# Performance work log

Hardware: AMD Instinct MI355X
Metric: run time of the kernel (lower is better)

## Reference

```python
import jax, jax.numpy as jnp
import numpy as np

B, C, P, H, W, S = 4, 256, 128, 56, 56, 5
EPS = 1e-5


def setup_inputs() -> dict:
    key = jax.random.key(0)
    ks = jax.random.split(key, 6)
    return {
        "x": jax.random.normal(ks[0], (B, C, H, W), jnp.float32),
        "Wt": jax.random.normal(ks[1], (P, C), jnp.float32) * 0.05,
        "Wp": jax.random.normal(ks[2], (P, C), jnp.float32) * 0.05,
        "Wg": jax.random.normal(ks[3], (S, P, C), jnp.float32) * 0.05,
        "W1": jax.random.normal(ks[4], (S, C, P), jnp.float32) * 0.05,
        "W2": jax.random.normal(ks[5], (S, C, P), jnp.float32) * 0.05,
        "gamma": jnp.ones((S, C), jnp.float32),
        "beta": jnp.zeros((S, C), jnp.float32),
    }


def _batchnorm(o, g, b):
    # training-mode BN over (batch, spatial); o: [b, C, n]
    mean = o.mean(axis=(0, 2), keepdims=True)
    var = ((o - mean) ** 2).mean(axis=(0, 2), keepdims=True)
    return (o - mean) * jax.lax.rsqrt(var + EPS) * g[None, :, None] + b[None, :, None]


def reference(x, Wt, Wp, Wg, W1, W2, gamma, beta):
    b, c, h, w = x.shape
    n = h * w
    xf = x.reshape(b, c, n)
    # 1x1 conv projections == channel matmuls
    t = jax.nn.relu(jnp.einsum('pc,bcn->bpn', Wt, xf))  # is_norm branch uses relu
    p = jax.nn.relu(jnp.einsum('pc,bcn->bpn', Wp, xf))
    att = jnp.einsum('bpi,bpj->bij', t, p)              # [b, n, n] affinity
    att = 0.5 * (att + jnp.swapaxes(att, 1, 2))         # is_sys symmetrization
    d = att.sum(axis=2)                                  # degree [b, n]
    d_safe = jnp.where(d != 0, d, 1.0)
    d_inv = jnp.where(d != 0, jax.lax.rsqrt(d_safe), 0.0)
    att = att * d_inv[:, None, :] * d_inv[:, :, None]    # D^-1/2 A D^-1/2
    out = xf
    for s in range(S):  # fixed small stage count
        g = jnp.einsum('pc,bcn->bpn', Wg[s], out)        # [b, P, n]
        ag = jnp.einsum('bij,bpj->bpi', att, g)          # att @ g over spatial
        o = jnp.einsum('cp,bpn->bcn', W1[s], ag) + jnp.einsum('cp,bpn->bcn', W2[s], g)
        out = _batchnorm(o, gamma[s], beta[s]) + out     # BN + residual
    return out.reshape(b, c, h, w)
```

## Files before the change

kernel.cpp:

```cpp
#include <hip/hip_runtime.h>

namespace {

constexpr int Bc = 4;
constexpr int Cc = 256;
constexpr int Pc = 128;
constexpr int Nc = 3136;
constexpr int Sc = 5;
constexpr int KSn = 7;
constexpr int KCH = 448;
constexpr float EPSc = 1e-5f;

typedef __attribute__((ext_vector_type(8))) short bf16x8;
typedef __attribute__((ext_vector_type(4))) float f32x4;
typedef __attribute__((ext_vector_type(8))) unsigned short u16x8;
typedef __attribute__((ext_vector_type(4))) unsigned short u16x4;

__device__ inline float bf2f(unsigned short u) {
    return __uint_as_float(((unsigned)u) << 16);
}
__device__ inline unsigned short f2bf(float f) {
    unsigned u = __float_as_uint(f);
    return (unsigned short)((u + 0x7FFFu + ((u >> 16) & 1u)) >> 16);
}

template <int EPI, int CMOUT, bool SPLITK, int BNSTAT, bool F32OUT>
__global__ __launch_bounds__(256) void mgemm(
    const unsigned short* __restrict__ A, int lda, long aB,
    const unsigned short* __restrict__ Bw, int ldb, long bB,
    unsigned short* __restrict__ outSM, int ldsm, long smB, long smSlice,
    unsigned short* __restrict__ outCM, long cmB,
    float* __restrict__ ps, float* __restrict__ ps2,
    int K, int kchunk, const float* __restrict__ dinv)
{
    constexpr int TBA = 64 * 64 * 2;
    constexpr int TBB = 128 * 64 * 2;
    constexpr int BUF = TBA + TBB;
    __shared__ __align__(16) char lds[2 * BUF];

    int b, kstart, kend;
    long smOff;
    if (SPLITK) {
        b = blockIdx.z & 3;
        int ks = blockIdx.z >> 2;
        kstart = ks * kchunk;
        kend = kstart + kchunk;
        smOff = (long)ks * smSlice;
    } else {
        b = blockIdx.z; kstart = 0; kend = K; smOff = 0;
    }
    const int n0 = blockIdx.x * 128;
    const int m0 = blockIdx.y * 64;
    const int tid = threadIdx.x;
    const int w = tid >> 6, l = tid & 63;

    const unsigned short* Ab = A + (size_t)b * aB + (size_t)m0 * lda;
    const unsigned short* Bb = Bw + (size_t)b * bB + (size_t)n0 * ldb;

    const int srow = w * 8 + (l >> 3);
    const int gsw = ((l & 7) ^ (l >> 3)) * 8;

    f32x4 acc[4][2] = {};

    auto stage = [&](int buf, int k0) {
        char* base = lds + buf * BUF;
#pragma unroll
        for (int j = 0; j < 2; ++j) {
            __builtin_amdgcn_global_load_lds(
                (const __attribute__((address_space(1))) void*)
                    (Ab + (size_t)(j * 32 + srow) * lda + k0 + gsw),
                (__attribute__((address_space(3))) void*)(base + j * 4096 + w * 1024),
                16, 0, 0);
        }
#pragma unroll
        for (int j = 0; j < 4; ++j) {
            __builtin_amdgcn_global_load_lds(
                (const __attribute__((address_space(1))) void*)
                    (Bb + (size_t)(j * 32 + srow) * ldb + k0 + gsw),
                (__attribute__((address_space(3))) void*)(base + TBA + j * 4096 + w * 1024),
                16, 0, 0);
        }
    };

    auto compute = [&](int buf) {
        const char* base = lds + buf * BUF;
        const int lo = l & 15, gq = l >> 4;
#pragma unroll
        for (int kh = 0; kh < 2; ++kh) {
            const int lg = kh * 4 + gq;
            bf16x8 bf[2];
#pragma unroll
            for (int c = 0; c < 2; ++c) {
                int brow = w * 32 + c * 16 + lo;
                bf[c] = *(const bf16x8*)(base + TBA + brow * 128 + ((lg ^ (brow & 7)) << 4));
            }
#pragma unroll
            for (int r = 0; r < 4; ++r) {
                int row = r * 16 + lo;
                bf16x8 af = *(const bf16x8*)(base + row * 128 + ((lg ^ (row & 7)) << 4));
                acc[r][0] = __builtin_amdgcn_mfma_f32_16x16x32_bf16(af, bf[0], acc[r][0], 0, 0, 0);
                acc[r][1] = __builtin_amdgcn_mfma_f32_16x16x32_bf16(af, bf[1], acc[r][1], 0, 0, 0);
            }
        }
    };

    stage(0, kstart);
    __syncthreads();
    const int nst = (kend - kstart) >> 6;
    for (int s = 0; s < nst; ++s) {
        if (s + 1 < nst) stage((s + 1) & 1, kstart + ((s + 1) << 6));
        compute(s & 1);
        __syncthreads();
    }

    float* ot = (float*)lds;
    {
        const int lo = l & 15, gq = l >> 4;
#pragma unroll
        for (int r = 0; r < 4; ++r)
#pragma unroll
            for (int c = 0; c < 2; ++c)
#pragma unroll
                for (int j = 0; j < 4; ++j) {
                    float v = acc[r][c][j];
                    if (EPI == 1) v = fmaxf(v, 0.f);
                    ot[(r * 16 + gq * 4 + j) * 132 + w * 32 + c * 16 + lo] = v;
                }
    }
    __syncthreads();

    {
        const int r = tid >> 2, c0 = (tid & 3) * 32;
        if (F32OUT) {
            float* dst = (float*)outSM + (size_t)b * smB + smOff +
                         (size_t)(m0 + r) * ldsm + n0 + c0;
#pragma unroll
            for (int k = 0; k < 8; ++k) {
                float4 v;
                v.x = ot[r * 132 + c0 + 4 * k + 0];
                v.y = ot[r * 132 + c0 + 4 * k + 1];
                v.z = ot[r * 132 + c0 + 4 * k + 2];
                v.w = ot[r * 132 + c0 + 4 * k + 3];
                *(float4*)(dst + 4 * k) = v;
            }
        } else {
            float sc = 1.f;
            if (EPI == 2) sc = 0.5f * dinv[(size_t)b * Nc + m0 + r];
            unsigned short* dst = outSM + (size_t)b * smB + smOff +
                                  (size_t)(m0 + r) * ldsm + n0 + c0;
#pragma unroll
            for (int k = 0; k < 4; ++k) {
                u16x8 o;
#pragma unroll
                for (int j = 0; j < 8; ++j) {
                    float v = ot[r * 132 + c0 + 8 * k + j];
                    if (EPI == 2) v *= sc;
                    o[j] = f2bf(v);
                }
                *(u16x8*)(dst + 8 * k) = o;
            }
        }
    }

    if (CMOUT) {
        const int c = tid >> 1, r0 = (tid & 1) * 32;
        const float* dv = dinv + (size_t)b * Nc + m0 + r0;
        unsigned short* dst = outCM + (size_t)b * cmB + (size_t)(n0 + c) * Nc + m0 + r0;
#pragma unroll
        for (int k = 0; k < 4; ++k) {
            u16x8 o;
#pragma unroll
            for (int j = 0; j < 8; ++j) {
                float v = ot[(r0 + 8 * k + j) * 132 + c];
                if (CMOUT == 2) v *= dv[8 * k + j];
                o[j] = f2bf(v);
            }
            *(u16x8*)(dst + 8 * k) = o;
        }
    }

    if (BNSTAT) {
        float* p1 = (float*)(lds + 35840);
        float* p2 = p1 + 256;
        const int col = tid & 127, half = tid >> 7;
        float s = 0.f, s2 = 0.f;
#pragma unroll
        for (int i = 0; i < 32; ++i) {
            float v = ot[(half * 32 + i) * 132 + col];
            s += v;
            if (BNSTAT == 2) s2 = fmaf(v, v, s2);
        }
        p1[half * 128 + col] = s;
        if (BNSTAT == 2) p2[half * 128 + col] = s2;
        __syncthreads();
        if (tid < 128) {
            float a = p1[tid] + p1[128 + tid];
            size_t slot = ((size_t)b * 49 + blockIdx.y) * 256 + n0 + tid;
            ps[slot] = a;
            if (BNSTAT == 2) ps2[slot] = p2[tid] + p2[128 + tid];
        }
    }
}

__global__ __launch_bounds__(256) void cvtw_k(
    const float* __restrict__ Wt, const float* __restrict__ Wp,
    const float* __restrict__ Wg, const float* __restrict__ W1,
    const float* __restrict__ W2,
    unsigned short* __restrict__ Wcomb, unsigned short* __restrict__ Wgh,
    unsigned short* __restrict__ Wcat)
{
    size_t e = ((size_t)blockIdx.x * 256 + threadIdx.x) * 4;
    const float* src; unsigned short* dst;
    if (e < 32768)      { src = Wt + e;           dst = Wcomb + e; }
    else if (e < 65536) { src = Wp + (e - 32768); dst = Wcomb + e; }
    else if (e < 65536 + 163840) {
        size_t o = e - 65536; src = Wg + o; dst = Wgh + o;
    } else if (e < 65536 + 2 * 163840) {
        size_t o = e - 65536 - 163840; src = W1 + o;
        dst = Wcat + ((o >> 7) << 8) + (o & 127);
    } else {
        size_t o = e - 65536 - 327680; src = W2 + o;
        dst = Wcat + ((o >> 7) << 8) + 128 + (o & 127);
    }
    float4 v = *(const float4*)src;
    u16x4 t;
    t[0] = f2bf(v.x); t[1] = f2bf(v.y); t[2] = f2bf(v.z); t[3] = f2bf(v.w);
    *(u16x4*)dst = t;
}

__global__ __launch_bounds__(256) void xpin_k(
    const float* __restrict__ x, float* __restrict__ out_sm,
    unsigned short* __restrict__ outh)
{
    __shared__ float tb[64][65];
    int b = blockIdx.z, c0 = blockIdx.y * 64, n0 = blockIdx.x * 64;
    int t = threadIdx.x;
    {
        int ci = t >> 2, nb = (t & 3) * 16;
        const float* src = x + ((size_t)b * Cc + c0 + ci) * Nc + n0 + nb;
#pragma unroll
        for (int k = 0; k < 4; ++k) {
            float4 v = *(const float4*)(src + 4 * k);
            tb[ci][nb + 4 * k + 0] = v.x; tb[ci][nb + 4 * k + 1] = v.y;
            tb[ci][nb + 4 * k + 2] = v.z; tb[ci][nb + 4 * k + 3] = v.w;
        }
    }
    __syncthreads();
    {
        int r = t >> 2, cb = (t & 3) * 16;
        size_t off = ((size_t)b * Nc + n0 + r) * Cc + c0 + cb;
        float vv[16];
#pragma unroll
        for (int j = 0; j < 16; ++j) vv[j] = tb[cb + j][r];
        float* dst = out_sm + off;
#pragma unroll
        for (int k = 0; k < 4; ++k) {
            float4 v; v.x = vv[4*k]; v.y = vv[4*k+1]; v.z = vv[4*k+2]; v.w = vv[4*k+3];
            *(float4*)(dst + 4 * k) = v;
        }
        u16x8 h1, h2;
#pragma unroll
        for (int j = 0; j < 8; ++j) { h1[j] = f2bf(vv[j]); h2[j] = f2bf(vv[8 + j]); }
        unsigned short* dh = outh + off;
        *(u16x8*)dh = h1;
        *(u16x8*)(dh + 8) = h2;
    }
}

__global__ __launch_bounds__(256) void xpout_k(
    const float* __restrict__ out_sm, float* __restrict__ outp)
{
    __shared__ float tb[64][65];
    int b = blockIdx.z, c0 = blockIdx.y * 64, n0 = blockIdx.x * 64;
    int t = threadIdx.x;
    {
        int r = t >> 2, cb = (t & 3) * 16;
        const float* src = out_sm + ((size_t)b * Nc + n0 + r) * Cc + c0 + cb;
#pragma unroll
        for (int k = 0; k < 4; ++k) {
            float4 v = *(const float4*)(src + 4 * k);
            tb[r][cb + 4 * k + 0] = v.x; tb[r][cb + 4 * k + 1] = v.y;
            tb[r][cb + 4 * k + 2] = v.z; tb[r][cb + 4 * k + 3] = v.w;
        }
    }
    __syncthreads();
    {
        int c = t >> 2, rb = (t & 3) * 16;
        float vv[16];
#pragma unroll
        for (int j = 0; j < 16; ++j) vv[j] = tb[rb + j][c];
        float* dst = outp + ((size_t)b * Cc + c0 + c) * Nc + n0 + rb;
#pragma unroll
        for (int k = 0; k < 4; ++k) {
            float4 v; v.x = vv[4*k]; v.y = vv[4*k+1]; v.z = vv[4*k+2]; v.w = vv[4*k+3];
            *(float4*)(dst + 4 * k) = v;
        }
    }
}

__global__ __launch_bounds__(256) void dinv_k(
    const unsigned short* __restrict__ U, const float* __restrict__ rp,
    float* __restrict__ dinv)
{
    __shared__ float rsl[256];
    int b = blockIdx.y, tid = threadIdx.x;
    float s = 0.f;
    for (int j = 0; j < 49; ++j) s += rp[((size_t)b * 49 + j) * 256 + tid];
    rsl[tid ^ 128] = s;
    __syncthreads();
    int i = blockIdx.x * 256 + tid;
    if (i < Nc) {
        const unsigned short* row = U + ((size_t)b * Nc + i) * 256;
        float acc = 0.f;
        for (int q0 = 0; q0 < 256; q0 += 8) {
            u16x8 v = *(const u16x8*)(row + q0);
#pragma unroll
            for (int j = 0; j < 8; ++j) acc = fmaf(bf2f(v[j]), rsl[q0 + j], acc);
        }
        float d = 0.5f * acc;
        dinv[(size_t)b * Nc + i] = d > 0.f ? rsqrtf(d) : 0.f;
    }
}

__global__ __launch_bounds__(256) void redmst_k(
    const float* __restrict__ Cpart, unsigned short* __restrict__ MstT)
{
    int e8 = blockIdx.x * 256 + threadIdx.x;
    int bp = e8 >> 5, qc = e8 & 31;
    size_t dstOff = ((size_t)bp * 32 + qc) * 8;
    size_t srcOff = ((size_t)bp * 32 + (qc ^ 16)) * 8;
    float4 s0 = {0.f, 0.f, 0.f, 0.f}, s1 = {0.f, 0.f, 0.f, 0.f};
    for (int ks = 0; ks < KSn; ++ks) {
        const float* base = Cpart + (size_t)ks * (Bc * Pc * Cc) + srcOff;
        float4 v0 = *(const float4*)base;
        float4 v1 = *(const float4*)(base + 4);
        s0.x += v0.x; s0.y += v0.y; s0.z += v0.z; s0.w += v0.w;
        s1.x += v1.x; s1.y += v1.y; s1.z += v1.z; s1.w += v1.w;
    }
    u16x8 o;
    o[0] = f2bf(s0.x); o[1] = f2bf(s0.y); o[2] = f2bf(s0.z); o[3] = f2bf(s0.w);
    o[4] = f2bf(s1.x); o[5] = f2bf(s1.y); o[6] = f2bf(s1.z); o[7] = f2bf(s1.w);
    *(u16x8*)(MstT + dstOff) = o;
}

__global__ __launch_bounds__(256) void bnfin_k(
    const float* __restrict__ ps, const float* __restrict__ ps2,
    const float* __restrict__ gamma, const float* __restrict__ beta,
    float* __restrict__ scale, float* __restrict__ shift)
{
    __shared__ float l1[256], l2[256];
    int t = threadIdx.x;
    int c = blockIdx.x * 16 + (t & 15);
    int gl = t >> 4;
    float a = 0.f, a2 = 0.f;
    for (int g = gl; g < 196; g += 16) {
        a += ps[(size_t)g * 256 + c];
        a2 += ps2[(size_t)g * 256 + c];
    }
    l1[t] = a; l2[t] = a2;
    __syncthreads();
    if (gl == 0) {
#pragma unroll
        for (int j = 1; j < 16; ++j) {
            a += l1[j * 16 + (t & 15)];
            a2 += l2[j * 16 + (t & 15)];
        }
        const float inv = 1.f / (float)(Bc * Nc);
        float mean = a * inv;
        float var = a2 * inv - mean * mean;
        float sc = gamma[c] * rsqrtf(var + EPSc);
        scale[c] = sc;
        shift[c] = beta[c] - mean * sc;
    }
}

__global__ __launch_bounds__(256) void bnapp_k(
    const unsigned short* __restrict__ o, const float* __restrict__ scale,
    const float* __restrict__ shift, float* __restrict__ out_sm,
    unsigned short* __restrict__ outh)
{
    __shared__ float lsc[256], lsh[256];
    int t = threadIdx.x;
    lsc[t] = scale[t];
    lsh[t] = shift[t];
    __syncthreads();
    size_t e = ((size_t)blockIdx.x * 256 + t) * 8;
    int c8 = (int)(e & 255);
    u16x8 ov = *(const u16x8*)(o + e);
    float* op = out_sm + e;
    float4 o1 = *(float4*)op, o2 = *(float4*)(op + 4);
    float r[8];
#pragma unroll
    for (int j = 0; j < 8; ++j) r[j] = fmaf(bf2f(ov[j]), lsc[c8 + j], lsh[c8 + j]);
    o1.x += r[0]; o1.y += r[1]; o1.z += r[2]; o1.w += r[3];
    o2.x += r[4]; o2.y += r[5]; o2.z += r[6]; o2.w += r[7];
    *(float4*)op = o1;
    *(float4*)(op + 4) = o2;
    u16x8 hv;
    hv[0] = f2bf(o1.x); hv[1] = f2bf(o1.y); hv[2] = f2bf(o1.z); hv[3] = f2bf(o1.w);
    hv[4] = f2bf(o2.x); hv[5] = f2bf(o2.y); hv[6] = f2bf(o2.z); hv[7] = f2bf(o2.w);
    *(u16x8*)(outh + e) = hv;
}

}

extern "C" void kernel_launch(void* const* d_in, const int* in_sizes, int n_in,
                              void* d_out, int out_size, void* d_ws, size_t ws_size,
                              hipStream_t stream) {
    const float* x     = (const float*)d_in[0];
    const float* Wt    = (const float*)d_in[1];
    const float* Wp    = (const float*)d_in[2];
    const float* Wg    = (const float*)d_in[3];
    const float* W1    = (const float*)d_in[4];
    const float* W2    = (const float*)d_in[5];
    const float* gamma = (const float*)d_in[6];
    const float* beta  = (const float*)d_in[7];

    char* p = (char*)d_ws;
    auto alloc = [&](size_t bytes) { char* r = p; p += (bytes + 255) & ~(size_t)255; return r; };
    float*          out_sm = (float*)         alloc((size_t)Bc * Nc * Cc * 4);
    unsigned short* outh   = (unsigned short*)alloc((size_t)Bc * Nc * Cc * 2);
    unsigned short* U_sm   = (unsigned short*)alloc((size_t)Bc * Nc * 256 * 2);
    unsigned short* U_cm   = (unsigned short*)alloc((size_t)Bc * 256 * Nc * 2);
    unsigned short* agg    = (unsigned short*)alloc((size_t)Bc * Nc * 256 * 2);
    unsigned short* g_cmd  = (unsigned short*)alloc((size_t)Bc * Pc * Nc * 2);
    unsigned short* o_sm   = (unsigned short*)alloc((size_t)Bc * Nc * Cc * 2);
    float*          Cpart  = (float*)         alloc((size_t)KSn * Bc * Pc * Cc * 4);
    unsigned short* MstT   = (unsigned short*)alloc((size_t)Bc * Pc * Cc * 2);
    unsigned short* Wcomb  = (unsigned short*)alloc((size_t)Cc * Cc * 2);
    unsigned short* Wgh    = (unsigned short*)alloc((size_t)Sc * Pc * Cc * 2);
    unsigned short* Wcat   = (unsigned short*)alloc((size_t)Sc * Cc * 256 * 2);
    float*          rp     = (float*)         alloc((size_t)Bc * 49 * 256 * 4);
    float*          dinv   = (float*)         alloc((size_t)Bc * Nc * 4);
    float*          ps     = (float*)         alloc((size_t)196 * 256 * 4);
    float*          ps2    = (float*)         alloc((size_t)196 * 256 * 4);
    float*          scale  = (float*)         alloc(256 * 4);
    float*          shiftb = (float*)         alloc(256 * 4);

    const long NC256 = (long)Nc * 256;
    dim3 blk(256);

    cvtw_k<<<544, blk, 0, stream>>>(Wt, Wp, Wg, W1, W2, Wcomb, Wgh, Wcat);
    xpin_k<<<dim3(49, 4, Bc), blk, 0, stream>>>(x, out_sm, outh);

    mgemm<1, 1, false, 1, false><<<dim3(2, 49, Bc), blk, 0, stream>>>(
        outh, 256, NC256, Wcomb, 256, 0,
        U_sm, 256, NC256, 0, U_cm, (long)256 * Nc, rp, nullptr, 256, 0, nullptr);

    dinv_k<<<dim3(13, Bc), blk, 0, stream>>>(U_sm, rp, dinv);

    for (int s = 0; s < Sc; ++s) {
        mgemm<0, 2, false, 0, false><<<dim3(1, 49, Bc), blk, 0, stream>>>(
            outh, 256, NC256, Wgh + (size_t)s * Pc * Cc, 256, 0,
            agg + 128, 256, NC256, 0, g_cmd, (long)Pc * Nc, nullptr, nullptr,
            256, 0, dinv);
        mgemm<0, 0, true, 0, true><<<dim3(2, 2, KSn * Bc), blk, 0, stream>>>(
            g_cmd, Nc, (long)Pc * Nc, U_cm, Nc, (long)256 * Nc,
            (unsigned short*)Cpart, 256, (long)Pc * Cc, (long)Bc * Pc * Cc,
            nullptr, 0, nullptr, nullptr, Nc, KCH, nullptr);
        redmst_k<<<64, blk, 0, stream>>>(Cpart, MstT);
        mgemm<2, 0, false, 0, false><<<dim3(1, 49, Bc), blk, 0, stream>>>(
            U_sm, 256, NC256, MstT, 256, (long)Pc * Cc,
            agg, 256, NC256, 0, nullptr, 0, nullptr, nullptr, 256, 0, dinv);
        mgemm<0, 0, false, 2, false><<<dim3(2, 49, Bc), blk, 0, stream>>>(
            agg, 256, NC256, Wcat + (size_t)s * Cc * 256, 256, 0,
            o_sm, 256, NC256, 0, nullptr, 0, ps, ps2, 256, 0, nullptr);
        bnfin_k<<<16, blk, 0, stream>>>(ps, ps2, gamma + s * Cc, beta + s * Cc,
                                        scale, shiftb);
        bnapp_k<<<1568, blk, 0, stream>>>(o_sm, scale, shiftb, out_sm, outh);
    }

    xpout_k<<<dim3(49, 4, Bc), blk, 0, stream>>>(out_sm, (float*)d_out);
}
```

Measured before the change: 280.0 us.

## Fuse BN-apply into next stage GEMM prologue, pad N, use 128-row tiles

Removes the standalone BN-apply kernel. The scale, shift and residual add now happen in the next stage's g-projection GEMM, which loads o and the residual, writes the updated residual and stages the bf16 A tile into LDS itself. The final stage's BN is folded into the output transpose. The spatial dimension is padded to 3200 so tiles divide evenly, the split-K count drops from 7 to 5, and the wide GEMMs use 128-row tiles to halve the grid and amortize B loads. In exchange, padding adds some wasted work, and the fused prologue puts synchronous global loads in the GEMM pipeline.

```diff
diff --git a/kernel.cpp b/kernel.cpp
--- a/kernel.cpp
+++ b/kernel.cpp
@@ -5,10 +5,11 @@
 constexpr int Bc = 4;
 constexpr int Cc = 256;
 constexpr int Pc = 128;
-constexpr int Nc = 3136;
+constexpr int NcT = 3136;
+constexpr int Np = 3200;
 constexpr int Sc = 5;
-constexpr int KSn = 7;
-constexpr int KCH = 448;
+constexpr int KSn = 5;
+constexpr int KCH = 640;
 constexpr float EPSc = 1e-5f;
 
 typedef __attribute__((ext_vector_type(8))) short bf16x8;
@@ -24,19 +25,24 @@
     return (unsigned short)((u + 0x7FFFu + ((u >> 16) & 1u)) >> 16);
 }
 
-template <int EPI, int CMOUT, bool SPLITK, int BNSTAT, bool F32OUT>
+template <int MT, int EPI, int CMOUT, bool SPLITK, int BNSTAT, bool F32OUT,
+          bool FUSEBN>
 __global__ __launch_bounds__(256) void mgemm(
     const unsigned short* __restrict__ A, int lda, long aB,
     const unsigned short* __restrict__ Bw, int ldb, long bB,
     unsigned short* __restrict__ outSM, int ldsm, long smB, long smSlice,
     unsigned short* __restrict__ outCM, long cmB,
     float* __restrict__ ps, float* __restrict__ ps2,
-    int K, int kchunk, const float* __restrict__ dinv)
-{
-    constexpr int TBA = 64 * 64 * 2;
+    int K, int kchunk, const float* __restrict__ dinv,
+    const unsigned short* __restrict__ oin, const float* __restrict__ bnsc,
+    const float* __restrict__ bnsh, float* __restrict__ resid)
+{
+    constexpr int TBA = MT * 64 * 2;
     constexpr int TBB = 128 * 64 * 2;
     constexpr int BUF = TBA + TBB;
-    __shared__ __align__(16) char lds[2 * BUF];
+    constexpr int OTB = MT * 132 * 4;
+    constexpr int LDSZ = (2 * BUF > OTB + 2048) ? 2 * BUF : (OTB + 2048);
+    __shared__ __align__(16) char lds[LDSZ];
 
     int b, kstart, kend;
     long smOff;
@@ -50,35 +56,87 @@
         b = blockIdx.z; kstart = 0; kend = K; smOff = 0;
     }
     const int n0 = blockIdx.x * 128;
-    const int m0 = blockIdx.y * 64;
+    const int m0 = blockIdx.y * MT;
     const int tid = threadIdx.x;
     const int w = tid >> 6, l = tid & 63;
 
     const unsigned short* Ab = A + (size_t)b * aB + (size_t)m0 * lda;
     const unsigned short* Bb = Bw + (size_t)b * bB + (size_t)n0 * ldb;
 
-    const int srow = w * 8 + (l >> 3);
-    const int gsw = ((l & 7) ^ (l >> 3)) * 8;
-
-    f32x4 acc[4][2] = {};
-
-    auto stage = [&](int buf, int k0) {
+    const int srow8 = tid >> 3;
+    const int sgran = tid & 7;
+    const int sswz = (sgran ^ (srow8 & 7)) * 8;
+    constexpr int AR = MT / 32;
+
+    constexpr int WC = (MT == 128) ? 2 : 4;
+    constexpr int NB = 128 / WC / 16;
+    const int wr = w / WC, wc = w % WC;
+
+    f32x4 acc[4][NB] = {};
+    float fup[AR][8];
+
+    auto stageA = [&](int buf, int k0) {
         char* base = lds + buf * BUF;
 #pragma unroll
-        for (int j = 0; j < 2; ++j) {
+        for (int j = 0; j < AR; ++j)
             __builtin_amdgcn_global_load_lds(
                 (const __attribute__((address_space(1))) void*)
-                    (Ab + (size_t)(j * 32 + srow) * lda + k0 + gsw),
-                (__attribute__((address_space(3))) void*)(base + j * 4096 + w * 1024),
+                    (Ab + (size_t)(j * 32 + srow8) * lda + k0 + sswz),
+                (__attribute__((address_space(3))) void*)(base + j * 4096 + tid * 16),
                 16, 0, 0);
-        }
-#pragma unroll
-        for (int j = 0; j < 4; ++j) {
+    };
+    auto stageB = [&](int buf, int k0) {
+        char* base = lds + buf * BUF + TBA;
+#pragma unroll
+        for (int j = 0; j < 4; ++j)
             __builtin_amdgcn_global_load_lds(
                 (const __attribute__((address_space(1))) void*)
-                    (Bb + (size_t)(j * 32 + srow) * ldb + k0 + gsw),
-                (__attribute__((address_space(3))) void*)(base + TBA + j * 4096 + w * 1024),
+                    (Bb + (size_t)(j * 32 + srow8) * ldb + k0 + sswz),
+                (__attribute__((address_space(3))) void*)(base + j * 4096 + tid * 16),
                 16, 0, 0);
+    };
+    auto fbLoad = [&](int k0) {
+        const float* scp = bnsc + k0 + sgran * 8;
+        const float* shp = bnsh + k0 + sgran * 8;
+        float4 s0 = *(const float4*)scp, s1 = *(const float4*)(scp + 4);
+        float4 h0 = *(const float4*)shp, h1 = *(const float4*)(shp + 4);
+#pragma unroll
+        for (int j = 0; j < AR; ++j) {
+            int row = j * 32 + srow8;
+            int n = m0 + row;
+            size_t off = ((size_t)b * Np + n) * 256 + k0 + sgran * 8;
+            if (n < NcT) {
+                u16x8 ov = *(const u16x8*)(oin + off);
+                float4 r0 = *(const float4*)(resid + off);
+                float4 r1 = *(const float4*)(resid + off + 4);
+                fup[j][0] = r0.x + fmaf(bf2f(ov[0]), s0.x, h0.x);
+                fup[j][1] = r0.y + fmaf(bf2f(ov[1]), s0.y, h0.y);
+                fup[j][2] = r0.z + fmaf(bf2f(ov[2]), s0.z, h0.z);
+                fup[j][3] = r0.w + fmaf(bf2f(ov[3]), s0.w, h0.w);
+                fup[j][4] = r1.x + fmaf(bf2f(ov[4]), s1.x, h1.x);
+                fup[j][5] = r1.y + fmaf(bf2f(ov[5]), s1.y, h1.y);
+                fup[j][6] = r1.z + fmaf(bf2f(ov[6]), s1.z, h1.z);
+                fup[j][7] = r1.w + fmaf(bf2f(ov[7]), s1.w, h1.w);
+            } else {
+#pragma unroll
+                for (int i = 0; i < 8; ++i) fup[j][i] = 0.f;
+            }
+            float4 w0, w1;
+            w0.x = fup[j][0]; w0.y = fup[j][1]; w0.z = fup[j][2]; w0.w = fup[j][3];
+            w1.x = fup[j][4]; w1.y = fup[j][5]; w1.z = fup[j][6]; w1.w = fup[j][7];
+            *(float4*)(resid + off) = w0;
+            *(float4*)(resid + off + 4) = w1;
+        }
+    };
+    auto fbWrite = [&](int buf) {
+        char* base = lds + buf * BUF;
+#pragma unroll
+        for (int j = 0; j < AR; ++j) {
+            int row = j * 32 + srow8;
+            u16x8 hv;
+#pragma unroll
+            for (int i = 0; i < 8; ++i) hv[i] = f2bf(fup[j][i]);
+            *(u16x8*)(base + row * 128 + ((sgran ^ (row & 7)) << 4)) = hv;
         }
     };
 
@@ -88,29 +146,53 @@
 #pragma unroll
         for (int kh = 0; kh < 2; ++kh) {
             const int lg = kh * 4 + gq;
-            bf16x8 bf[2];
-#pragma unroll
-            for (int c = 0; c < 2; ++c) {
-                int brow = w * 32 + c * 16 + lo;
-                bf[c] = *(const bf16x8*)(base + TBA + brow * 128 + ((lg ^ (brow & 7)) << 4));
+            bf16x8 bf[NB];
+#pragma unroll
+            for (int c = 0; c < NB; ++c) {
+                int brow = wc * (16 * NB) + c * 16 + lo;
+                bf[c] = *(const bf16x8*)(base + TBA + brow * 128 +
+                                         ((lg ^ (brow & 7)) << 4));
             }
 #pragma unroll
             for (int r = 0; r < 4; ++r) {
-                int row = r * 16 + lo;
-                bf16x8 af = *(const bf16x8*)(base + row * 128 + ((lg ^ (row & 7)) << 4));
-                acc[r][0] = __builtin_amdgcn_mfma_f32_16x16x32_bf16(af, bf[0], acc[r][0], 0, 0, 0);
-                acc[r][1] = __builtin_amdgcn_mfma_f32_16x16x32_bf16(af, bf[1], acc[r][1], 0, 0, 0);
+                int arow = wr * 64 + r * 16 + lo;
+                bf16x8 af = *(const bf16x8*)(base + arow * 128 +
+                                             ((lg ^ (arow & 7)) << 4));
+#pragma unroll
+                for (int c = 0; c < NB; ++c)
+                    acc[r][c] = __builtin_amdgcn_mfma_f32_16x16x32_bf16(
+                        af, bf[c], acc[r][c], 0, 0, 0);
             }
         }
     };
 
-    stage(0, kstart);
-    __syncthreads();
     const int nst = (kend - kstart) >> 6;
-    for (int s = 0; s < nst; ++s) {
-        if (s + 1 < nst) stage((s + 1) & 1, kstart + ((s + 1) << 6));
-        compute(s & 1);
+    if constexpr (FUSEBN) {
+        fbLoad(kstart);
+        fbWrite(0);
+        stageB(0, kstart);
         __syncthreads();
+        for (int s = 0; s < nst; ++s) {
+            if (s + 1 < nst) {
+                fbLoad(kstart + ((s + 1) << 6));
+                stageB((s + 1) & 1, kstart + ((s + 1) << 6));
+            }
+            compute(s & 1);
+            if (s + 1 < nst) fbWrite((s + 1) & 1);
+            __syncthreads();
+        }
+    } else {
+        stageA(0, kstart);
+        stageB(0, kstart);
+        __syncthreads();
+        for (int s = 0; s < nst; ++s) {
+            if (s + 1 < nst) {
+                stageA((s + 1) & 1, kstart + ((s + 1) << 6));
+                stageB((s + 1) & 1, kstart + ((s + 1) << 6));
+            }
+            compute(s & 1);
+            __syncthreads();
+        }
     }
 
     float* ot = (float*)lds;
@@ -119,23 +201,26 @@
 #pragma unroll
         for (int r = 0; r < 4; ++r)
 #pragma unroll
-            for (int c = 0; c < 2; ++c)
+            for (int c = 0; c < NB; ++c)
 #pragma unroll
                 for (int j = 0; j < 4; ++j) {
                     float v = acc[r][c][j];
                     if (EPI == 1) v = fmaxf(v, 0.f);
-                    ot[(r * 16 + gq * 4 + j) * 132 + w * 32 + c * 16 + lo] = v;
+                    ot[(wr * 64 + r * 16 + gq * 4 + j) * 132 +
+                       wc * (16 * NB) + c * 16 + lo] = v;
                 }
     }
     __syncthreads();
 
     {
-        const int r = tid >> 2, c0 = (tid & 3) * 32;
+        constexpr int TPR = 256 / MT;
+        const int r = tid / TPR;
+        const int c0 = (tid % TPR) * (MT / 2);
         if (F32OUT) {
             float* dst = (float*)outSM + (size_t)b * smB + smOff +
                          (size_t)(m0 + r) * ldsm + n0 + c0;
 #pragma unroll
-            for (int k = 0; k < 8; ++k) {
+            for (int k = 0; k < MT / 8; ++k) {
                 float4 v;
                 v.x = ot[r * 132 + c0 + 4 * k + 0];
                 v.y = ot[r * 132 + c0 + 4 * k + 1];
@@ -145,11 +230,11 @@
             }
         } else {
             float sc = 1.f;
-            if (EPI == 2) sc = 0.5f * dinv[(size_t)b * Nc + m0 + r];
+            if (EPI == 2) sc = 0.5f * dinv[(size_t)b * Np + m0 + r];
             unsigned short* dst = outSM + (size_t)b * smB + smOff +
                                   (size_t)(m0 + r) * ldsm + n0 + c0;
 #pragma unroll
-            for (int k = 0; k < 4; ++k) {
+            for (int k = 0; k < MT / 16; ++k) {
                 u16x8 o;
 #pragma unroll
                 for (int j = 0; j < 8; ++j) {
@@ -163,11 +248,12 @@
     }
 
     if (CMOUT) {
-        const int c = tid >> 1, r0 = (tid & 1) * 32;
-        const float* dv = dinv + (size_t)b * Nc + m0 + r0;
-        unsigned short* dst = outCM + (size_t)b * cmB + (size_t)(n0 + c) * Nc + m0 + r0;
-#pragma unroll
-        for (int k = 0; k < 4; ++k) {
+        const int c = tid >> 1, r0 = (tid & 1) * (MT / 2);
+        const float* dv = dinv + (size_t)b * Np + m0 + r0;
+        unsigned short* dst = outCM + (size_t)b * cmB + (size_t)(n0 + c) * Np +
+                              m0 + r0;
+#pragma unroll
+        for (int k = 0; k < MT / 16; ++k) {
             u16x8 o;
 #pragma unroll
             for (int j = 0; j < 8; ++j) {
@@ -180,13 +266,13 @@
     }
 
     if (BNSTAT) {
-        float* p1 = (float*)(lds + 35840);
+        float* p1 = (float*)(lds + OTB);
         float* p2 = p1 + 256;
         const int col = tid & 127, half = tid >> 7;
         float s = 0.f, s2 = 0.f;
 #pragma unroll
-        for (int i = 0; i < 32; ++i) {
-            float v = ot[(half * 32 + i) * 132 + col];
+        for (int i = 0; i < MT / 2; ++i) {
+            float v = ot[(half * (MT / 2) + i) * 132 + col];
             s += v;
             if (BNSTAT == 2) s2 = fmaf(v, v, s2);
         }
@@ -195,7 +281,7 @@
         __syncthreads();
         if (tid < 128) {
             float a = p1[tid] + p1[128 + tid];
-            size_t slot = ((size_t)b * 49 + blockIdx.y) * 256 + n0 + tid;
+            size_t slot = ((size_t)b * gridDim.y + blockIdx.y) * 256 + n0 + tid;
             ps[slot] = a;
             if (BNSTAT == 2) ps2[slot] = p2[tid] + p2[128 + tid];
         }
@@ -235,9 +321,10 @@
     __shared__ float tb[64][65];
     int b = blockIdx.z, c0 = blockIdx.y * 64, n0 = blockIdx.x * 64;
     int t = threadIdx.x;
-    {
+    const bool pad = (n0 >= NcT);
+    if (!pad) {
         int ci = t >> 2, nb = (t & 3) * 16;
-        const float* src = x + ((size_t)b * Cc + c0 + ci) * Nc + n0 + nb;
+        const float* src = x + ((size_t)b * Cc + c0 + ci) * NcT + n0 + nb;
 #pragma unroll
         for (int k = 0; k < 4; ++k) {
             float4 v = *(const float4*)(src + 4 * k);
@@ -246,41 +333,52 @@
         }
     }
     __syncthreads();
+    int r = t >> 2, cb = (t & 3) * 16;
+    size_t off = ((size_t)b * Np + n0 + r) * 256 + c0 + cb;
+    float vv[16];
+#pragma unroll
+    for (int j = 0; j < 16; ++j) vv[j] = pad ? 0.f : tb[cb + j][r];
+    float* dst = out_sm + off;
+#pragma unroll
+    for (int k = 0; k < 4; ++k) {
+        float4 v; v.x = vv[4*k]; v.y = vv[4*k+1]; v.z = vv[4*k+2]; v.w = vv[4*k+3];
+        *(float4*)(dst + 4 * k) = v;
+    }
+    u16x8 h1, h2;
+#pragma unroll
+    for (int j = 0; j < 8; ++j) { h1[j] = f2bf(vv[j]); h2[j] = f2bf(vv[8 + j]); }
+    unsigned short* dh = outh + off;
+    *(u16x8*)dh = h1;
+    *(u16x8*)(dh + 8) = h2;
+}
+
+__global__ __launch_bounds__(256) void xpoutbn_k(
+    const float* __restrict__ out_sm, const unsigned short* __restrict__ oin,
+    const float* __restrict__ scale, const float* __restrict__ shift,
+    float* __restrict__ outp)
+{
+    __shared__ float tb[64][65];
+    __shared__ float lsc[64], lsh[64];
+    int b = blockIdx.z, c0 = blockIdx.y * 64, n0 = blockIdx.x * 64;
+    int t = threadIdx.x;
+    if (t < 64) { lsc[t] = scale[c0 + t]; lsh[t] = shift[c0 + t]; }
+    __syncthreads();
     {
         int r = t >> 2, cb = (t & 3) * 16;
-        size_t off = ((size_t)b * Nc + n0 + r) * Cc + c0 + cb;
-        float vv[16];
-#pragma unroll
-        for (int j = 0; j < 16; ++j) vv[j] = tb[cb + j][r];
-        float* dst = out_sm + off;
-#pragma unroll
-        for (int k = 0; k < 4; ++k) {
-            float4 v; v.x = vv[4*k]; v.y = vv[4*k+1]; v.z = vv[4*k+2]; v.w = vv[4*k+3];
-            *(float4*)(dst + 4 * k) = v;
-        }
-        u16x8 h1, h2;
-#pragma unroll
-        for (int j = 0; j < 8; ++j) { h1[j] = f2bf(vv[j]); h2[j] = f2bf(vv[8 + j]); }
-        unsigned short* dh = outh + off;
-        *(u16x8*)dh = h1;
-        *(u16x8*)(dh + 8) = h2;
-    }
-}
-
-__global__ __launch_bounds__(256) void xpout_k(
-    const float* __restrict__ out_sm, float* __restrict__ outp)
-{
-    __shared__ float tb[64][65];
-    int b = blockIdx.z, c0 = blockIdx.y * 64, n0 = blockIdx.x * 64;
-    int t = threadIdx.x;
-    {
-        int r = t >> 2, cb = (t & 3) * 16;
-        const float* src = out_sm + ((size_t)b * Nc + n0 + r) * Cc + c0 + cb;
-#pragma unroll
-        for (int k = 0; k < 4; ++k) {
-            float4 v = *(const float4*)(src + 4 * k);
-            tb[r][cb + 4 * k + 0] = v.x; tb[r][cb + 4 * k + 1] = v.y;
-            tb[r][cb + 4 * k + 2] = v.z; tb[r][cb + 4 * k + 3] = v.w;
+        size_t off = ((size_t)b * Np + n0 + r) * 256 + c0 + cb;
+#pragma unroll
+        for (int k = 0; k < 2; ++k) {
+            float4 a0 = *(const float4*)(out_sm + off + 8 * k);
+            float4 a1 = *(const float4*)(out_sm + off + 8 * k + 4);
+            u16x8 ov = *(const u16x8*)(oin + off + 8 * k);
+            tb[r][cb + 8*k + 0] = a0.x + fmaf(bf2f(ov[0]), lsc[cb + 8*k + 0], lsh[cb + 8*k + 0]);
+            tb[r][cb + 8*k + 1] = a0.y + fmaf(bf2f(ov[1]), lsc[cb + 8*k + 1], lsh[cb + 8*k + 1]);
+            tb[r][cb + 8*k + 2] = a0.z + fmaf(bf2f(ov[2]), lsc[cb + 8*k + 2], lsh[cb + 8*k + 2]);
+            tb[r][cb + 8*k + 3] = a0.w + fmaf(bf2f(ov[3]), lsc[cb + 8*k + 3], lsh[cb + 8*k + 3]);
+            tb[r][cb + 8*k + 4] = a1.x + fmaf(bf2f(ov[4]), lsc[cb + 8*k + 4], lsh[cb + 8*k + 4]);
+            tb[r][cb + 8*k + 5] = a1.y + fmaf(bf2f(ov[5]), lsc[cb + 8*k + 5], lsh[cb + 8*k + 5]);
+            tb[r][cb + 8*k + 6] = a1.z + fmaf(bf2f(ov[6]), lsc[cb + 8*k + 6], lsh[cb + 8*k + 6]);
+            tb[r][cb + 8*k + 7] = a1.w + fmaf(bf2f(ov[7]), lsc[cb + 8*k + 7], lsh[cb + 8*k + 7]);
         }
     }
     __syncthreads();
@@ -289,7 +387,7 @@
         float vv[16];
 #pragma unroll
         for (int j = 0; j < 16; ++j) vv[j] = tb[rb + j][c];
-        float* dst = outp + ((size_t)b * Cc + c0 + c) * Nc + n0 + rb;
+        float* dst = outp + ((size_t)b * Cc + c0 + c) * NcT + n0 + rb;
 #pragma unroll
         for (int k = 0; k < 4; ++k) {
             float4 v; v.x = vv[4*k]; v.y = vv[4*k+1]; v.z = vv[4*k+2]; v.w = vv[4*k+3];
@@ -305,12 +403,12 @@
     __shared__ float rsl[256];
     int b = blockIdx.y, tid = threadIdx.x;
     float s = 0.f;
-    for (int j = 0; j < 49; ++j) s += rp[((size_t)b * 49 + j) * 256 + tid];
+    for (int j = 0; j < 25; ++j) s += rp[((size_t)b * 25 + j) * 256 + tid];
     rsl[tid ^ 128] = s;
     __syncthreads();
     int i = blockIdx.x * 256 + tid;
-    if (i < Nc) {
-        const unsigned short* row = U + ((size_t)b * Nc + i) * 256;
+    if (i < Np) {
+        const unsigned short* row = U + ((size_t)b * Np + i) * 256;
         float acc = 0.f;
         for (int q0 = 0; q0 < 256; q0 += 8) {
             u16x8 v = *(const u16x8*)(row + q0);
@@ -318,7 +416,7 @@
             for (int j = 0; j < 8; ++j) acc = fmaf(bf2f(v[j]), rsl[q0 + j], acc);
         }
         float d = 0.5f * acc;
-        dinv[(size_t)b * Nc + i] = d > 0.f ? rsqrtf(d) : 0.f;
+        dinv[(size_t)b * Np + i] = d > 0.f ? rsqrtf(d) : 0.f;
     }
 }
 
@@ -353,7 +451,7 @@
     int c = blockIdx.x * 16 + (t & 15);
     int gl = t >> 4;
     float a = 0.f, a2 = 0.f;
-    for (int g = gl; g < 196; g += 16) {
+    for (int g = gl; g < 100; g += 16) {
         a += ps[(size_t)g * 256 + c];
         a2 += ps2[(size_t)g * 256 + c];
     }
@@ -365,41 +463,13 @@
             a += l1[j * 16 + (t & 15)];
             a2 += l2[j * 16 + (t & 15)];
         }
-        const float inv = 1.f / (float)(Bc * Nc);
+        const float inv = 1.f / (float)(Bc * NcT);
         float mean = a * inv;
         float var = a2 * inv - mean * mean;
         float sc = gamma[c] * rsqrtf(var + EPSc);
         scale[c] = sc;
         shift[c] = beta[c] - mean * sc;
     }
-}
-
-__global__ __launch_bounds__(256) void bnapp_k(
-    const unsigned short* __restrict__ o, const float* __restrict__ scale,
-    const float* __restrict__ shift, float* __restrict__ out_sm,
-    unsigned short* __restrict__ outh)
-{
-    __shared__ float lsc[256], lsh[256];
-    int t = threadIdx.x;
-    lsc[t] = scale[t];
-    lsh[t] = shift[t];
-    __syncthreads();
-    size_t e = ((size_t)blockIdx.x * 256 + t) * 8;
-    int c8 = (int)(e & 255);
-    u16x8 ov = *(const u16x8*)(o + e);
-    float* op = out_sm + e;
-    float4 o1 = *(float4*)op, o2 = *(float4*)(op + 4);
-    float r[8];
-#pragma unroll
-    for (int j = 0; j < 8; ++j) r[j] = fmaf(bf2f(ov[j]), lsc[c8 + j], lsh[c8 + j]);
-    o1.x += r[0]; o1.y += r[1]; o1.z += r[2]; o1.w += r[3];
-    o2.x += r[4]; o2.y += r[5]; o2.z += r[6]; o2.w += r[7];
-    *(float4*)op = o1;
-    *(float4*)(op + 4) = o2;
-    u16x8 hv;
-    hv[0] = f2bf(o1.x); hv[1] = f2bf(o1.y); hv[2] = f2bf(o1.z); hv[3] = f2bf(o1.w);
-    hv[4] = f2bf(o2.x); hv[5] = f2bf(o2.y); hv[6] = f2bf(o2.z); hv[7] = f2bf(o2.w);
-    *(u16x8*)(outh + e) = hv;
 }
 
 }
@@ -418,57 +488,67 @@
 
     char* p = (char*)d_ws;
     auto alloc = [&](size_t bytes) { char* r = p; p += (bytes + 255) & ~(size_t)255; return r; };
-    float*          out_sm = (float*)         alloc((size_t)Bc * Nc * Cc * 4);
-    unsigned short* outh   = (unsigned short*)alloc((size_t)Bc * Nc * Cc * 2);
-    unsigned short* U_sm   = (unsigned short*)alloc((size_t)Bc * Nc * 256 * 2);
-    unsigned short* U_cm   = (unsigned short*)alloc((size_t)Bc * 256 * Nc * 2);
-    unsigned short* agg    = (unsigned short*)alloc((size_t)Bc * Nc * 256 * 2);
-    unsigned short* g_cmd  = (unsigned short*)alloc((size_t)Bc * Pc * Nc * 2);
-    unsigned short* o_sm   = (unsigned short*)alloc((size_t)Bc * Nc * Cc * 2);
+    float*          out_sm = (float*)         alloc((size_t)Bc * Np * 256 * 4);
+    unsigned short* outh   = (unsigned short*)alloc((size_t)Bc * Np * 256 * 2);
+    unsigned short* U_sm   = (unsigned short*)alloc((size_t)Bc * Np * 256 * 2);
+    unsigned short* U_cm   = (unsigned short*)alloc((size_t)Bc * 256 * Np * 2);
+    unsigned short* agg    = (unsigned short*)alloc((size_t)Bc * Np * 256 * 2);
+    unsigned short* g_cmd  = (unsigned short*)alloc((size_t)Bc * Pc * Np * 2);
+    unsigned short* o_sm   = (unsigned short*)alloc((size_t)Bc * Np * 256 * 2);
     float*          Cpart  = (float*)         alloc((size_t)KSn * Bc * Pc * Cc * 4);
     unsigned short* MstT   = (unsigned short*)alloc((size_t)Bc * Pc * Cc * 2);
     unsigned short* Wcomb  = (unsigned short*)alloc((size_t)Cc * Cc * 2);
     unsigned short* Wgh    = (unsigned short*)alloc((size_t)Sc * Pc * Cc * 2);
     unsigned short* Wcat   = (unsigned short*)alloc((size_t)Sc * Cc * 256 * 2);
-    float*          rp     = (float*)         alloc((size_t)Bc * 49 * 256 * 4);
-    float*          dinv   = (float*)         alloc((size_t)Bc * Nc * 4);
-    float*          ps     = (float*)         alloc((size_t)196 * 256 * 4);
-    float*          ps2    = (float*)         alloc((size_t)196 * 256 * 4);
+    float*          rp     = (float*)         alloc((size_t)100 * 256 * 4);
+    float*          dinv   = (float*)         alloc((size_t)Bc * Np * 4);
+    float*          ps     = (float*)         alloc((size_t)100 * 256 * 4);
+    float*          ps2    = (float*)         alloc((size_t)100 * 256 * 4);
     float*          scale  = (float*)         alloc(256 * 4);
     float*          shiftb = (float*)         alloc(256 * 4);
 
-    const long NC256 = (long)Nc * 256;
+    const long NpC = (long)Np * 256;
     dim3 blk(256);
 
     cvtw_k<<<544, blk, 0, stream>>>(Wt, Wp, Wg, W1, W2, Wcomb, Wgh, Wcat);
-    xpin_k<<<dim3(49, 4, Bc), blk, 0, stream>>>(x, out_sm, outh);
-
-    mgemm<1, 1, false, 1, false><<<dim3(2, 49, Bc), blk, 0, stream>>>(
-        outh, 256, NC256, Wcomb, 256, 0,
-        U_sm, 256, NC256, 0, U_cm, (long)256 * Nc, rp, nullptr, 256, 0, nullptr);
+    xpin_k<<<dim3(50, 4, Bc), blk, 0, stream>>>(x, out_sm, outh);
+
+    mgemm<128, 1, 1, false, 1, false, false><<<dim3(2, 25, Bc), blk, 0, stream>>>(
+        outh, 256, NpC, Wcomb, 256, 0,
+        U_sm, 256, NpC, 0, U_cm, (long)256 * Np, rp, nullptr,
+        256, 0, nullptr, nullptr, nullptr, nullptr, nullptr);
 
     dinv_k<<<dim3(13, Bc), blk, 0, stream>>>(U_sm, rp, dinv);
 
     for (int s = 0; s < Sc; ++s) {
-        mgemm<0, 2, false, 0, false><<<dim3(1, 49, Bc), blk, 0, stream>>>(
-            outh, 256, NC256, Wgh + (size_t)s * Pc * Cc, 256, 0,
-            agg + 128, 256, NC256, 0, g_cmd, (long)Pc * Nc, nullptr, nullptr,
-            256, 0, dinv);
-        mgemm<0, 0, true, 0, true><<<dim3(2, 2, KSn * Bc), blk, 0, stream>>>(
-            g_cmd, Nc, (long)Pc * Nc, U_cm, Nc, (long)256 * Nc,
+        if (s == 0)
+            mgemm<64, 0, 2, false, 0, false, false><<<dim3(1, 50, Bc), blk, 0, stream>>>(
+                outh, 256, NpC, Wgh, 256, 0,
+                agg + 128, 256, NpC, 0, g_cmd, (long)Pc * Np, nullptr, nullptr,
+                256, 0, dinv, nullptr, nullptr, nullptr, nullptr);
+        else
+            mgemm<64, 0, 2, false, 0, false, true><<<dim3(1, 50, Bc), blk, 0, stream>>>(
+                outh, 256, NpC, Wgh + (size_t)s * Pc * Cc, 256, 0,
+                agg + 128, 256, NpC, 0, g_cmd, (long)Pc * Np, nullptr, nullptr,
+                256, 0, dinv, o_sm, scale, shiftb, out_sm);
+        mgemm<64, 0, 0, true, 0, true, false><<<dim3(2, 2, KSn * Bc), blk, 0, stream>>>(
+            g_cmd, Np, (long)Pc * Np, U_cm, Np, (long)256 * Np,
             (unsigned short*)Cpart, 256, (long)Pc * Cc, (long)Bc * Pc * Cc,
-            nullptr, 0, nullptr, nullptr, Nc, KCH, nullptr);
+            nullptr, 0, nullptr, nullptr, Np, KCH, nullptr,
+            nullptr, nullptr, nullptr, nullptr);
         redmst_k<<<64, blk, 0, stream>>>(Cpart, MstT);
-        mgemm<2, 0, false, 0, false><<<dim3(1, 49, Bc), blk, 0, stream>>>(
-            U_sm, 256, NC256, MstT, 256, (long)Pc * Cc,
-            agg, 256, NC256, 0, nullptr, 0, nullptr, nullptr, 256, 0, dinv);
-        mgemm<0, 0, false, 2, false><<<dim3(2, 49, Bc), blk, 0, stream>>>(
-            agg, 256, NC256, Wcat + (size_t)s * Cc * 256, 256, 0,
-            o_sm, 256, NC256, 0, nullptr, 0, ps, ps2, 256, 0, nullptr);
+        mgemm<64, 2, 0, false, 0, false, false><<<dim3(1, 50, Bc), blk, 0, stream>>>(
+            U_sm, 256, NpC, MstT, 256, (long)Pc * Cc,
+            agg, 256, NpC, 0, nullptr, 0, nullptr, nullptr,
+            256, 0, dinv, nullptr, nullptr, nullptr, nullptr);
+        mgemm<128, 0, 0, false, 2, false, false><<<dim3(2, 25, Bc), blk, 0, stream>>>(
+            agg, 256, NpC, Wcat + (size_t)s * Cc * 256, 256, 0,
+            o_sm, 256, NpC, 0, nullptr, 0, ps, ps2,
+            256, 0, nullptr, nullptr, nullptr, nullptr, nullptr);
         bnfin_k<<<16, blk, 0, stream>>>(ps, ps2, gamma + s * Cc, beta + s * Cc,
                                         scale, shiftb);
-        bnapp_k<<<1568, blk, 0, stream>>>(o_sm, scale, shiftb, out_sm, outh);
-    }
-
-    xpout_k<<<dim3(49, 4, Bc), blk, 0, stream>>>(out_sm, (float*)d_out);
-}
+    }
+
+    xpoutbn_k<<<dim3(49, 4, Bc), blk, 0, stream>>>(out_sm, o_sm, scale, shiftb,
+                                                   (float*)d_out);
+}
```

Result: faster. 264.9 us (-5.4%).
